# Kernel tuning notes

Measured on AMD Instinct MI355X. Metric: run time of the kernel, lower is better.

The kernel has to match this reference:

```python
import jax, jax.numpy as jnp
import numpy as np

EPS = 1e-3  # keras LayerNormalization default epsilon


def _ln(x, g, b):
    m = jnp.mean(x, axis=-1, keepdims=True)
    v = jnp.mean(jnp.square(x - m), axis=-1, keepdims=True)
    return (x - m) * jax.lax.rsqrt(v + EPS) * g + b


def setup_inputs() -> dict:
    key = jax.random.key(0)
    B, T, C, H = 64, 256, 1024, 16
    D = C // H
    ks = jax.random.split(key, 16)
    s = 0.02
    return {
        "x": jax.random.normal(ks[0], (B, T, C), jnp.float32),
        # per-head q/k/v projections (no bias), stacked over heads [H, C, D]
        "wq": jax.random.normal(ks[1], (H, C, D), jnp.float32) * s,
        "wk": jax.random.normal(ks[2], (H, C, D), jnp.float32) * s,
        "wv": jax.random.normal(ks[3], (H, C, D), jnp.float32) * s,
        "w_proj": jax.random.normal(ks[4], (C, C), jnp.float32) * s,
        "b_proj": jnp.zeros((C,), jnp.float32),
        # FFN: C -> 4C (relu) -> C
        "w1": jax.random.normal(ks[5], (C, 4 * C), jnp.float32) * s,
        "b1": jnp.zeros((4 * C,), jnp.float32),
        "w2": jax.random.normal(ks[6], (4 * C, C), jnp.float32) * s,
        "b2": jnp.zeros((C,), jnp.float32),
        # LayerNorm params: ln1 (pre-attn), ln2 (pre-ffn), ln3 (inside FeedForward)
        "g1": jnp.ones((C,), jnp.float32), "be1": jnp.zeros((C,), jnp.float32),
        "g2": jnp.ones((C,), jnp.float32), "be2": jnp.zeros((C,), jnp.float32),
        "g3": jnp.ones((C,), jnp.float32), "be3": jnp.zeros((C,), jnp.float32),
    }


def reference(x, wq, wk, wv, w_proj, b_proj, w1, b1, w2, b2,
              g1, be1, g2, be2, g3, be3):
    B, T, C = x.shape
    # --- multi-head causal self-attention on LN1(x) ---
    h = _ln(x, g1, be1)
    q = jnp.einsum('btc,hcd->bhtd', h, wq)
    k = jnp.einsum('btc,hcd->bhtd', h, wk)
    v = jnp.einsum('btc,hcd->bhtd', h, wv)
    # NOTE: original scales by C**-0.5 with C = n_embd (full dim), not head_size
    scores = jnp.einsum('bhtd,bhsd->bhts', q, k) * (C ** -0.5)
    causal = jnp.tril(jnp.ones((T, T), dtype=bool))
    scores = jnp.where(causal, scores, -jnp.inf)
    attn = jax.nn.softmax(scores, axis=-1)  # dropout is identity at inference
    out = jnp.einsum('bhts,bhsd->bhtd', attn, v)
    out = out.transpose(0, 2, 1, 3).reshape(B, T, C)  # concat heads
    out = out @ w_proj + b_proj
    x = x + out
    # --- FeedForward block (contains its own residual + LayerNorm) ---
    y = _ln(x, g2, be2)
    z = jax.nn.relu(y @ w1 + b1) @ w2 + b2
    return x + _ln(y + z, g3, be3)
```

## Files before the change

kernel.cpp:

```cpp
#include <hip/hip_runtime.h>

typedef __bf16 bf16_t;
typedef __bf16 bf16x8 __attribute__((ext_vector_type(8)));
typedef float f32x4 __attribute__((ext_vector_type(4)));

#define LN_EPS 1e-3f

__device__ __forceinline__ void gload_lds16(const void* g, void* l) {
    __builtin_amdgcn_global_load_lds(
        (__attribute__((address_space(1))) void*)(g),
        (__attribute__((address_space(3))) void*)(l), 16, 0, 0);
}

__global__ __launch_bounds__(256)
void transpose_f32_bf16(const float* __restrict__ in, bf16_t* __restrict__ outp,
                        int ldi, int ldo)
{
    __shared__ float tile[64][65];
    const int k0 = blockIdx.x * 64, n0 = blockIdx.y * 64;
    const int tid = threadIdx.x;
    const int r = tid >> 2;
    const int q = tid & 3;
    const float* src = in + (long)(k0 + r) * ldi + n0 + q * 16;
#pragma unroll
    for (int j = 0; j < 4; ++j) {
        float4 v = *(const float4*)(src + j * 4);
        tile[r][q * 16 + j * 4 + 0] = v.x;
        tile[r][q * 16 + j * 4 + 1] = v.y;
        tile[r][q * 16 + j * 4 + 2] = v.z;
        tile[r][q * 16 + j * 4 + 3] = v.w;
    }
    __syncthreads();
    union { bf16_t e[16]; uint4 u[2]; } pk;
#pragma unroll
    for (int j = 0; j < 16; ++j) pk.e[j] = (bf16_t)tile[q * 16 + j][r];
    bf16_t* dst = outp + (long)(n0 + r) * ldo + k0 + q * 16;
    *(uint4*)(dst)     = pk.u[0];
    *(uint4*)(dst + 8) = pk.u[1];
}

__global__ __launch_bounds__(256)
void pack_qkv_t(const float* __restrict__ wq, const float* __restrict__ wk,
                const float* __restrict__ wv, bf16_t* __restrict__ outp)
{
    __shared__ float tile[64][65];
    const int m   = blockIdx.y;
    const int sel = m >> 4, h = m & 15;
    const float* in = ((sel == 0) ? wq : (sel == 1) ? wk : wv) + (long)h * 65536;
    bf16_t* out = outp + ((long)sel * 1024 + h * 64) * 1024;
    const int k0 = blockIdx.x * 64;
    const int tid = threadIdx.x;
    const int r = tid >> 2;
    const int q = tid & 3;
    const float* src = in + (long)(k0 + r) * 64 + q * 16;
#pragma unroll
    for (int j = 0; j < 4; ++j) {
        float4 v = *(const float4*)(src + j * 4);
        tile[r][q * 16 + j * 4 + 0] = v.x;
        tile[r][q * 16 + j * 4 + 1] = v.y;
        tile[r][q * 16 + j * 4 + 2] = v.z;
        tile[r][q * 16 + j * 4 + 3] = v.w;
    }
    __syncthreads();
    union { bf16_t e[16]; uint4 u[2]; } pk;
#pragma unroll
    for (int j = 0; j < 16; ++j) pk.e[j] = (bf16_t)tile[q * 16 + j][r];
    bf16_t* dst = out + (long)r * 1024 + k0 + q * 16;
    *(uint4*)(dst)     = pk.u[0];
    *(uint4*)(dst + 8) = pk.u[1];
}

__global__ __launch_bounds__(256)
void ln_fwd(const float* __restrict__ in, const float* __restrict__ g,
            const float* __restrict__ be, bf16_t* __restrict__ outp)
{
    const long row = blockIdx.x;
    const int t = threadIdx.x;
    float4 v = ((const float4*)(in + row * 1024))[t];
    float s  = v.x + v.y + v.z + v.w;
    float sq = v.x * v.x + v.y * v.y + v.z * v.z + v.w * v.w;
#pragma unroll
    for (int off = 1; off < 64; off <<= 1) {
        s  += __shfl_xor(s, off);
        sq += __shfl_xor(sq, off);
    }
    __shared__ float red[8];
    if ((t & 63) == 0) { red[(t >> 6) * 2] = s; red[(t >> 6) * 2 + 1] = sq; }
    __syncthreads();
    s  = red[0] + red[2] + red[4] + red[6];
    sq = red[1] + red[3] + red[5] + red[7];
    float mean = s * 0.0009765625f;
    float var  = sq * 0.0009765625f - mean * mean;
    float rstd = rsqrtf(var + LN_EPS);
    float4 gv = ((const float4*)g)[t];
    float4 bv = ((const float4*)be)[t];
    union { bf16_t h[4]; uint2 u; } pk;
    pk.h[0] = (bf16_t)((v.x - mean) * rstd * gv.x + bv.x);
    pk.h[1] = (bf16_t)((v.y - mean) * rstd * gv.y + bv.y);
    pk.h[2] = (bf16_t)((v.z - mean) * rstd * gv.z + bv.z);
    pk.h[3] = (bf16_t)((v.w - mean) * rstd * gv.w + bv.w);
    *(uint2*)(outp + row * 1024 + t * 4) = pk.u;
}

__global__ __launch_bounds__(256)
void ln3_kernel(const bf16_t* __restrict__ in, const float* __restrict__ g,
                const float* __restrict__ be, float* outp, const float* res)
{
    const long row = blockIdx.x;
    const int t = threadIdx.x;
    union { uint2 u; bf16_t h[4]; } pk;
    pk.u = *(const uint2*)(in + row * 1024 + t * 4);
    float v0 = (float)pk.h[0], v1 = (float)pk.h[1], v2 = (float)pk.h[2], v3 = (float)pk.h[3];
    float s  = v0 + v1 + v2 + v3;
    float sq = v0 * v0 + v1 * v1 + v2 * v2 + v3 * v3;
#pragma unroll
    for (int off = 1; off < 64; off <<= 1) {
        s  += __shfl_xor(s, off);
        sq += __shfl_xor(sq, off);
    }
    __shared__ float red[8];
    if ((t & 63) == 0) { red[(t >> 6) * 2] = s; red[(t >> 6) * 2 + 1] = sq; }
    __syncthreads();
    s  = red[0] + red[2] + red[4] + red[6];
    sq = red[1] + red[3] + red[5] + red[7];
    float mean = s * 0.0009765625f;
    float var  = sq * 0.0009765625f - mean * mean;
    float rstd = rsqrtf(var + LN_EPS);
    float4 gv = ((const float4*)g)[t];
    float4 bv = ((const float4*)be)[t];
    float4 rv = ((const float4*)(res + row * 1024))[t];
    float4 ov;
    ov.x = rv.x + (v0 - mean) * rstd * gv.x + bv.x;
    ov.y = rv.y + (v1 - mean) * rstd * gv.y + bv.y;
    ov.z = rv.z + (v2 - mean) * rstd * gv.z + bv.z;
    ov.w = rv.w + (v3 - mean) * rstd * gv.w + bv.w;
    ((float4*)outp)[row * 256 + t] = ov;
}

template<int MODE>
__global__ __launch_bounds__(512, 2)
void gemm_bt(const bf16_t* __restrict__ Ap, const bf16_t* __restrict__ Bp,
             void* outp, const float* __restrict__ bias,
             const void* addp, int M, int N, int K)
{
    __shared__ __attribute__((aligned(16))) bf16_t As0[256 * 64];
    __shared__ __attribute__((aligned(16))) bf16_t As1[256 * 64];
    __shared__ __attribute__((aligned(16))) bf16_t As2[256 * 64];
    __shared__ __attribute__((aligned(16))) bf16_t Bs0[256 * 64];
    __shared__ __attribute__((aligned(16))) bf16_t Bs1[256 * 64];

    const int tid  = threadIdx.x;
    const int w    = tid >> 6, lane = tid & 63;
    const int l16  = lane & 15, lg = lane >> 4;
    const int wm   = w >> 2, wn = w & 3;
    const int srow = lane >> 3;
    const int sslot = lane & 7;

    const int gx  = gridDim.x;
    const int gy  = gridDim.y;
    const int nwg = gx * gy;
    const int bid = blockIdx.y * gx + blockIdx.x;
    const int cpx = nwg >> 3;
    const int sid = (bid & 7) * cpx + (bid >> 3);
    const long m0 = (long)(sid / gy) * 256;
    const long n0 = (long)(sid % gy) * 256;
    const int nkt = K >> 6;

    f32x4 acc[8][4] = {};
    bf16x8 a[4][2], b0[2][2], b1[2][2];

    auto STAGEH = [&](const bf16_t* src, long row0, int kt, bf16_t* dst, int h) {
#pragma unroll
        for (int i = 0; i < 2; ++i) {
            int r  = h * 128 + w * 16 + i * 8 + srow;
            int ss = sslot ^ (r & 7);
            gload_lds16(src + (row0 + r) * (long)K + (long)kt * 64 + ss * 8,
                        dst + (h * 128 + w * 16 + i * 8) * 64);
        }
    };

#define LDA_M(buf, mh) do {                                               \
    _Pragma("unroll") for (int j = 0; j < 4; ++j)                         \
    _Pragma("unroll") for (int kk = 0; kk < 2; ++kk) {                    \
        int r  = wm * 128 + (mh) * 64 + j * 16 + l16;                     \
        int ss = (kk * 4 + lg) ^ (r & 7);                                 \
        a[j][kk] = *(const bf16x8*)&buf[r * 64 + ss * 8];                 \
    } } while (0)

#define LDB_M(dst, buf, nh) do {                                          \
    _Pragma("unroll") for (int n = 0; n < 2; ++n)                         \
    _Pragma("unroll") for (int kk = 0; kk < 2; ++kk) {                    \
        int r  = wn * 64 + ((nh) * 2 + n) * 16 + l16;                     \
        int ss = (kk * 4 + lg) ^ (r & 7);                                 \
        dst[n][kk] = *(const bf16x8*)&buf[r * 64 + ss * 8];               \
    } } while (0)

#define MMA_M(bv, mh, nh) do {                                            \
    __builtin_amdgcn_s_setprio(1);                                        \
    _Pragma("unroll") for (int j = 0; j < 4; ++j)                         \
    _Pragma("unroll") for (int n = 0; n < 2; ++n)                         \
    _Pragma("unroll") for (int kk = 0; kk < 2; ++kk)                      \
        acc[(mh) * 4 + j][(nh) * 2 + n] =                                 \
            __builtin_amdgcn_mfma_f32_16x16x32_bf16(                      \
                a[j][kk], bv[n][kk], acc[(mh) * 4 + j][(nh) * 2 + n],     \
                0, 0, 0);                                                 \
    __builtin_amdgcn_s_setprio(0);                                        \
} while (0)

#define PRE_MFMA() do { __builtin_amdgcn_s_barrier();                     \
    asm volatile("s_waitcnt lgkmcnt(0)" ::: "memory");                    \
    __builtin_amdgcn_sched_barrier(0); } while (0)

    STAGEH(Ap, m0, 0, As0, 0); STAGEH(Ap, m0, 0, As0, 1);
    STAGEH(Bp, n0, 0, Bs0, 0); STAGEH(Bp, n0, 0, Bs0, 1);
    if (nkt > 1) { STAGEH(Ap, m0, 1, As1, 0); STAGEH(Ap, m0, 1, As1, 1); }
    asm volatile("s_waitcnt vmcnt(0)" ::: "memory");
    __builtin_amdgcn_s_barrier();
    __builtin_amdgcn_sched_barrier(0);

    bf16_t *Ar = As0, *An1 = As1, *An2 = As2;
    bf16_t *Br = Bs0, *Bw = Bs1;

    for (int c = 0; c < nkt; ++c) {
        const bool pfa = (c + 2 < nkt);
        const bool pfb = (c + 1 < nkt);

        LDA_M(Ar, 0); LDB_M(b0, Br, 0);
        if (pfb) { STAGEH(Bp, n0, c + 1, Bw, 0); STAGEH(Bp, n0, c + 1, Bw, 1); }
        if (pfa) STAGEH(Ap, m0, c + 2, An2, 0);
        PRE_MFMA(); MMA_M(b0, 0, 0); __builtin_amdgcn_s_barrier();
        LDB_M(b1, Br, 1);
        PRE_MFMA(); MMA_M(b1, 0, 1); __builtin_amdgcn_s_barrier();
        LDA_M(Ar, 1);
        if (pfa) STAGEH(Ap, m0, c + 2, An2, 1);
        PRE_MFMA(); MMA_M(b1, 1, 1); __builtin_amdgcn_s_barrier();
        if (pfa) { asm volatile("s_waitcnt vmcnt(4)" ::: "memory"); }
        else     { asm volatile("s_waitcnt vmcnt(0)" ::: "memory"); }
        __builtin_amdgcn_s_barrier();
        __builtin_amdgcn_sched_barrier(0);
        MMA_M(b0, 1, 0); __builtin_amdgcn_s_barrier();

        bf16_t* t = Ar; Ar = An1; An1 = An2; An2 = t;
        t = Br; Br = Bw; Bw = t;
    }

#pragma unroll
    for (int fm = 0; fm < 8; ++fm) {
#pragma unroll
        for (int fn = 0; fn < 4; ++fn) {
            const long gcol = n0 + wn * 64 + fn * 16 + l16;
            float bv = 0.f;
            if (MODE != 0 && MODE != 4) bv = bias[gcol];
            const long grow0 = m0 + wm * 128 + fm * 16 + lg * 4;
            if (MODE == 4 && gcol >= 2048) {
                union { bf16_t h[4]; uint2 u; } pk;
#pragma unroll
                for (int e = 0; e < 4; ++e) pk.h[e] = (bf16_t)acc[fm][fn][e];
                const int hh = (int)(gcol >> 6) - 32;
                const int d  = (int)gcol & 63;
                const long bb = grow0 >> 8;
                const int s0  = (int)grow0 & 255;
                *(uint2*)((bf16_t*)addp + ((bb * 16 + hh) * 64 + d) * 256 + s0) = pk.u;
                continue;
            }
#pragma unroll
            for (int e = 0; e < 4; ++e) {
                const long grow = grow0 + e;
                float v = acc[fm][fn][e];
                if (MODE == 0 || MODE == 4) {
                    ((bf16_t*)outp)[grow * N + gcol] = (bf16_t)v;
                } else if (MODE == 1) {
                    v += bv + ((const float*)addp)[grow * N + gcol];
                    ((float*)outp)[grow * N + gcol] = v;
                } else if (MODE == 2) {
                    v += bv; v = v > 0.f ? v : 0.f;
                    ((bf16_t*)outp)[grow * N + gcol] = (bf16_t)v;
                } else {
                    v += bv + (float)((const bf16_t*)addp)[grow * N + gcol];
                    ((bf16_t*)outp)[grow * N + gcol] = (bf16_t)v;
                }
            }
        }
    }
#undef LDA_M
#undef LDB_M
#undef MMA_M
#undef PRE_MFMA
}

__global__ __launch_bounds__(256)
void attn_kernel(const bf16_t* __restrict__ qkv, const bf16_t* __restrict__ vt,
                 bf16_t* __restrict__ outp)
{
    __shared__ __attribute__((aligned(16))) bf16_t Kt[4][64 * 64];
    __shared__ __attribute__((aligned(16))) bf16_t Vt[4][64 * 64];
    __shared__ __attribute__((aligned(16))) bf16_t Ps[4][16 * 72];

    const int tid = threadIdx.x, w = tid >> 6, lane = tid & 63;
    const int l16 = lane & 15, lg = lane >> 4;
    const int b = blockIdx.x >> 4, hh = blockIdx.x & 15;
    const bf16_t* pq = qkv + (long)(b * 256) * 3072 + hh * 64;
    const bf16_t* pv = vt + (long)blockIdx.x * 64 * 256;
    const int sr8 = lane >> 3;
    const int sl  = lane & 7;

    bf16x8 qf[4][2];
#pragma unroll
    for (int fm = 0; fm < 4; ++fm)
#pragma unroll
        for (int kk = 0; kk < 2; ++kk)
            qf[fm][kk] = *(const bf16x8*)(pq + (long)(fm * 64 + w * 16 + l16) * 3072
                                          + kk * 32 + lg * 8);

#pragma unroll
    for (int st = 0; st < 4; ++st)
#pragma unroll
        for (int i = 0; i < 2; ++i) {
            int r  = w * 16 + i * 8 + sr8;
            int ss = sl ^ (r & 7);
            gload_lds16(pq + (long)(st * 64 + r) * 3072 + 1024 + ss * 8,
                        &Kt[st][(w * 16 + i * 8) * 64]);
            gload_lds16(pv + (long)r * 256 + st * 64 + ss * 8,
                        &Vt[st][(w * 16 + i * 8) * 64]);
        }
    asm volatile("s_waitcnt vmcnt(0)" ::: "memory");
    __syncthreads();

    f32x4 o[4][4] = {};
    float mrun[4][4], lrun[4][4];
#pragma unroll
    for (int i = 0; i < 4; ++i)
#pragma unroll
        for (int j = 0; j < 4; ++j) { mrun[i][j] = -__builtin_inff(); lrun[i][j] = 0.f; }

#pragma unroll
    for (int st = 0; st < 4; ++st) {
        f32x4 s[4][4] = {};
#pragma unroll
        for (int ks = 0; ks < 2; ++ks) {
            bf16x8 kb[4];
#pragma unroll
            for (int fs = 0; fs < 4; ++fs)
                kb[fs] = *(const bf16x8*)&Kt[st][(fs * 16 + l16) * 64
                                                + ((ks * 4 + lg) ^ (l16 & 7)) * 8];
#pragma unroll
            for (int fm = 0; fm < 4; ++fm) {
                if (fm < st) continue;
#pragma unroll
                for (int fs = 0; fs < 4; ++fs)
                    s[fm][fs] = __builtin_amdgcn_mfma_f32_16x16x32_bf16(
                        qf[fm][ks], kb[fs], s[fm][fs], 0, 0, 0);
            }
        }

#pragma unroll
        for (int fm = 0; fm < 4; ++fm) {
            if (fm < st) continue;
#pragma unroll
            for (int fs = 0; fs < 4; ++fs)
#pragma unroll
                for (int e = 0; e < 4; ++e) {
                    float v = s[fm][fs][e] * 0.03125f;
                    if (st == fm && (fs * 16 + l16) > (w * 16 + lg * 4 + e))
                        v = -__builtin_inff();
                    s[fm][fs][e] = v;
                }
#pragma unroll
            for (int e = 0; e < 4; ++e) {
                float pm = fmaxf(fmaxf(s[fm][0][e], s[fm][1][e]),
                                 fmaxf(s[fm][2][e], s[fm][3][e]));
#pragma unroll
                for (int off = 1; off < 16; off <<= 1) pm = fmaxf(pm, __shfl_xor(pm, off));
                float mnew  = fmaxf(mrun[fm][e], pm);
                float alpha = __expf(mrun[fm][e] - mnew);
                float rs = 0.f;
#pragma unroll
                for (int fs = 0; fs < 4; ++fs) {
                    float p = __expf(s[fm][fs][e] - mnew);
                    s[fm][fs][e] = p;
                    rs += p;
                }
#pragma unroll
                for (int off = 1; off < 16; off <<= 1) rs += __shfl_xor(rs, off);
                lrun[fm][e] = lrun[fm][e] * alpha + rs;
                mrun[fm][e] = mnew;
#pragma unroll
                for (int fd = 0; fd < 4; ++fd) o[fm][fd][e] *= alpha;
            }
#pragma unroll
            for (int fs = 0; fs < 4; ++fs)
#pragma unroll
                for (int e = 0; e < 4; ++e)
                    Ps[w][(lg * 4 + e) * 72 + fs * 16 + l16] = (bf16_t)s[fm][fs][e];
            bf16x8 ap0 = *(const bf16x8*)&Ps[w][l16 * 72 + lg * 8];
            bf16x8 ap1 = *(const bf16x8*)&Ps[w][l16 * 72 + 32 + lg * 8];
#pragma unroll
            for (int fd = 0; fd < 4; ++fd) {
                bf16x8 vb0 = *(const bf16x8*)&Vt[st][(fd * 16 + l16) * 64
                                                    + ((lg) ^ (l16 & 7)) * 8];
                bf16x8 vb1 = *(const bf16x8*)&Vt[st][(fd * 16 + l16) * 64
                                                    + ((4 + lg) ^ (l16 & 7)) * 8];
                o[fm][fd] = __builtin_amdgcn_mfma_f32_16x16x32_bf16(ap0, vb0, o[fm][fd], 0, 0, 0);
                o[fm][fd] = __builtin_amdgcn_mfma_f32_16x16x32_bf16(ap1, vb1, o[fm][fd], 0, 0, 0);
            }
        }
    }

#pragma unroll
    for (int fm = 0; fm < 4; ++fm)
#pragma unroll
        for (int e = 0; e < 4; ++e) {
            float inv = 1.f / lrun[fm][e];
            long row = (long)b * 256 + fm * 64 + w * 16 + lg * 4 + e;
#pragma unroll
            for (int fd = 0; fd < 4; ++fd)
                outp[row * 1024 + hh * 64 + fd * 16 + l16] =
                    (bf16_t)(o[fm][fd][e] * inv);
        }
}

extern "C" void kernel_launch(void* const* d_in, const int* in_sizes, int n_in,
                              void* d_out, int out_size, void* d_ws, size_t ws_size,
                              hipStream_t stream)
{
    (void)in_sizes; (void)n_in; (void)out_size; (void)ws_size;
    const float* x      = (const float*)d_in[0];
    const float* wq     = (const float*)d_in[1];
    const float* wk     = (const float*)d_in[2];
    const float* wv     = (const float*)d_in[3];
    const float* w_proj = (const float*)d_in[4];
    const float* b_proj = (const float*)d_in[5];
    const float* w1     = (const float*)d_in[6];
    const float* b1     = (const float*)d_in[7];
    const float* w2     = (const float*)d_in[8];
    const float* b2     = (const float*)d_in[9];
    const float* g1  = (const float*)d_in[10]; const float* be1 = (const float*)d_in[11];
    const float* g2  = (const float*)d_in[12]; const float* be2 = (const float*)d_in[13];
    const float* g3  = (const float*)d_in[14]; const float* be3 = (const float*)d_in[15];

    char* ws = (char*)d_ws;
    bf16_t* wqkv  = (bf16_t*)(ws + 0);
    bf16_t* wproj = (bf16_t*)(ws + 6291456);
    bf16_t* w1t   = (bf16_t*)(ws + 8388608);
    bf16_t* w2t   = (bf16_t*)(ws + 16777216);
    bf16_t* h     = (bf16_t*)(ws + 25165824);
    bf16_t* qkv   = (bf16_t*)(ws + 58720256);
    bf16_t* attn  = h;
    bf16_t* u     = h;
    bf16_t* y     = (bf16_t*)(ws + 159383552);
    bf16_t* vt    = y;
    float*  x2    = (float*)d_out;
    bf16_t* tbuf  = y;

    const int M = 16384;

    transpose_f32_bf16<<<dim3(16, 16), 256, 0, stream>>>(w_proj, wproj, 1024, 1024);
    transpose_f32_bf16<<<dim3(16, 64), 256, 0, stream>>>(w1, w1t, 4096, 1024);
    transpose_f32_bf16<<<dim3(64, 16), 256, 0, stream>>>(w2, w2t, 1024, 4096);
    pack_qkv_t<<<dim3(16, 48), 256, 0, stream>>>(wq, wk, wv, wqkv);

    ln_fwd<<<M, 256, 0, stream>>>(x, g1, be1, h);
    gemm_bt<4><<<dim3(64, 12), 512, 0, stream>>>(h, wqkv, qkv, nullptr, vt, M, 3072, 1024);
    attn_kernel<<<1024, 256, 0, stream>>>(qkv, vt, attn);
    gemm_bt<1><<<dim3(64, 4), 512, 0, stream>>>(attn, wproj, x2, b_proj, x, M, 1024, 1024);
    ln_fwd<<<M, 256, 0, stream>>>(x2, g2, be2, y);
    gemm_bt<2><<<dim3(64, 16), 512, 0, stream>>>(y, w1t, u, b1, nullptr, M, 4096, 1024);
    gemm_bt<3><<<dim3(64, 4), 512, 0, stream>>>(u, w2t, tbuf, b2, y, M, 1024, 4096);
    ln3_kernel<<<M, 256, 0, stream>>>(tbuf, g3, be3, (float*)d_out, x2);
}
```

Before: 623.4 us.

## Merge weight-prep kernels, store residual x2 in bf16, and reorder A prefetch

The four weight transpose/pack launches become one prep_w kernel that picks its tile from the block index. When the workspace is big enough, the attention-projection GEMM writes the residual sum x2 as bf16 into workspace rather than fp32 into the output. New bf16-input LN and LN3 variants then read it, cutting memory traffic for the mid-block residual. Separately, the second-half A prefetch in the GEMM main loop is issued one MFMA phase earlier to overlap it better. Keeping the residual in bf16 lowers the precision of the skip connection added to the final output.

```diff
diff --git a/kernel.cpp b/kernel.cpp
--- a/kernel.cpp
+++ b/kernel.cpp
@@ -12,62 +12,55 @@
         (__attribute__((address_space(3))) void*)(l), 16, 0, 0);
 }
 
-__global__ __launch_bounds__(256)
-void transpose_f32_bf16(const float* __restrict__ in, bf16_t* __restrict__ outp,
-                        int ldi, int ldo)
-{
-    __shared__ float tile[64][65];
-    const int k0 = blockIdx.x * 64, n0 = blockIdx.y * 64;
+__device__ __forceinline__ void tile_tr(const float* in, long ldi,
+                                        bf16_t* out, long ldo,
+                                        int k0, int n0, float* tile)
+{
     const int tid = threadIdx.x;
-    const int r = tid >> 2;
-    const int q = tid & 3;
+    const int r = tid >> 2, q = tid & 3;
     const float* src = in + (long)(k0 + r) * ldi + n0 + q * 16;
 #pragma unroll
     for (int j = 0; j < 4; ++j) {
         float4 v = *(const float4*)(src + j * 4);
-        tile[r][q * 16 + j * 4 + 0] = v.x;
-        tile[r][q * 16 + j * 4 + 1] = v.y;
-        tile[r][q * 16 + j * 4 + 2] = v.z;
-        tile[r][q * 16 + j * 4 + 3] = v.w;
+        tile[r * 65 + q * 16 + j * 4 + 0] = v.x;
+        tile[r * 65 + q * 16 + j * 4 + 1] = v.y;
+        tile[r * 65 + q * 16 + j * 4 + 2] = v.z;
+        tile[r * 65 + q * 16 + j * 4 + 3] = v.w;
     }
     __syncthreads();
     union { bf16_t e[16]; uint4 u[2]; } pk;
 #pragma unroll
-    for (int j = 0; j < 16; ++j) pk.e[j] = (bf16_t)tile[q * 16 + j][r];
-    bf16_t* dst = outp + (long)(n0 + r) * ldo + k0 + q * 16;
+    for (int j = 0; j < 16; ++j) pk.e[j] = (bf16_t)tile[(q * 16 + j) * 65 + r];
+    bf16_t* dst = out + (long)(n0 + r) * ldo + k0 + q * 16;
     *(uint4*)(dst)     = pk.u[0];
     *(uint4*)(dst + 8) = pk.u[1];
 }
 
 __global__ __launch_bounds__(256)
-void pack_qkv_t(const float* __restrict__ wq, const float* __restrict__ wk,
-                const float* __restrict__ wv, bf16_t* __restrict__ outp)
-{
-    __shared__ float tile[64][65];
-    const int m   = blockIdx.y;
-    const int sel = m >> 4, h = m & 15;
-    const float* in = ((sel == 0) ? wq : (sel == 1) ? wk : wv) + (long)h * 65536;
-    bf16_t* out = outp + ((long)sel * 1024 + h * 64) * 1024;
-    const int k0 = blockIdx.x * 64;
-    const int tid = threadIdx.x;
-    const int r = tid >> 2;
-    const int q = tid & 3;
-    const float* src = in + (long)(k0 + r) * 64 + q * 16;
-#pragma unroll
-    for (int j = 0; j < 4; ++j) {
-        float4 v = *(const float4*)(src + j * 4);
-        tile[r][q * 16 + j * 4 + 0] = v.x;
-        tile[r][q * 16 + j * 4 + 1] = v.y;
-        tile[r][q * 16 + j * 4 + 2] = v.z;
-        tile[r][q * 16 + j * 4 + 3] = v.w;
-    }
-    __syncthreads();
-    union { bf16_t e[16]; uint4 u[2]; } pk;
-#pragma unroll
-    for (int j = 0; j < 16; ++j) pk.e[j] = (bf16_t)tile[q * 16 + j][r];
-    bf16_t* dst = out + (long)r * 1024 + k0 + q * 16;
-    *(uint4*)(dst)     = pk.u[0];
-    *(uint4*)(dst + 8) = pk.u[1];
+void prep_w(const float* __restrict__ wq, const float* __restrict__ wk,
+            const float* __restrict__ wv, const float* __restrict__ w_proj,
+            const float* __restrict__ w1, const float* __restrict__ w2,
+            bf16_t* __restrict__ wqkv, bf16_t* __restrict__ wproj,
+            bf16_t* __restrict__ w1t, bf16_t* __restrict__ w2t)
+{
+    __shared__ float tile[64 * 65];
+    int id = blockIdx.x;
+    if (id < 256) {
+        tile_tr(w_proj, 1024, wproj, 1024, (id & 15) * 64, (id >> 4) * 64, tile);
+    } else if (id < 1280) {
+        int t = id - 256;
+        tile_tr(w1, 4096, w1t, 1024, (t & 15) * 64, (t >> 4) * 64, tile);
+    } else if (id < 2304) {
+        int t = id - 1280;
+        tile_tr(w2, 1024, w2t, 4096, (t & 63) * 64, (t >> 6) * 64, tile);
+    } else {
+        int t = id - 2304;
+        int m = t >> 4, kx = t & 15;
+        int sel = m >> 4, h = m & 15;
+        const float* in = ((sel == 0) ? wq : (sel == 1) ? wk : wv) + (long)h * 65536;
+        bf16_t* out = wqkv + ((long)sel * 1024 + h * 64) * 1024;
+        tile_tr(in, 64, out, 1024, kx * 64, 0, tile);
+    }
 }
 
 __global__ __launch_bounds__(256)
@@ -103,14 +96,15 @@
 }
 
 __global__ __launch_bounds__(256)
-void ln3_kernel(const bf16_t* __restrict__ in, const float* __restrict__ g,
-                const float* __restrict__ be, float* outp, const float* res)
+void ln_fwd_b(const bf16_t* __restrict__ in, const float* __restrict__ g,
+              const float* __restrict__ be, bf16_t* __restrict__ outp)
 {
     const long row = blockIdx.x;
     const int t = threadIdx.x;
-    union { uint2 u; bf16_t h[4]; } pk;
-    pk.u = *(const uint2*)(in + row * 1024 + t * 4);
-    float v0 = (float)pk.h[0], v1 = (float)pk.h[1], v2 = (float)pk.h[2], v3 = (float)pk.h[3];
+    union { uint2 u; bf16_t h[4]; } pin;
+    pin.u = *(const uint2*)(in + row * 1024 + t * 4);
+    float v0 = (float)pin.h[0], v1 = (float)pin.h[1],
+          v2 = (float)pin.h[2], v3 = (float)pin.h[3];
     float s  = v0 + v1 + v2 + v3;
     float sq = v0 * v0 + v1 * v1 + v2 * v2 + v3 * v3;
 #pragma unroll
@@ -128,12 +122,56 @@
     float rstd = rsqrtf(var + LN_EPS);
     float4 gv = ((const float4*)g)[t];
     float4 bv = ((const float4*)be)[t];
-    float4 rv = ((const float4*)(res + row * 1024))[t];
+    union { bf16_t h[4]; uint2 u; } pk;
+    pk.h[0] = (bf16_t)((v0 - mean) * rstd * gv.x + bv.x);
+    pk.h[1] = (bf16_t)((v1 - mean) * rstd * gv.y + bv.y);
+    pk.h[2] = (bf16_t)((v2 - mean) * rstd * gv.z + bv.z);
+    pk.h[3] = (bf16_t)((v3 - mean) * rstd * gv.w + bv.w);
+    *(uint2*)(outp + row * 1024 + t * 4) = pk.u;
+}
+
+template<int RESB>
+__global__ __launch_bounds__(256)
+void ln3_kernel(const bf16_t* __restrict__ in, const float* __restrict__ g,
+                const float* __restrict__ be, float* outp, const void* res)
+{
+    const long row = blockIdx.x;
+    const int t = threadIdx.x;
+    union { uint2 u; bf16_t h[4]; } pk;
+    pk.u = *(const uint2*)(in + row * 1024 + t * 4);
+    float v0 = (float)pk.h[0], v1 = (float)pk.h[1], v2 = (float)pk.h[2], v3 = (float)pk.h[3];
+    float s  = v0 + v1 + v2 + v3;
+    float sq = v0 * v0 + v1 * v1 + v2 * v2 + v3 * v3;
+#pragma unroll
+    for (int off = 1; off < 64; off <<= 1) {
+        s  += __shfl_xor(s, off);
+        sq += __shfl_xor(sq, off);
+    }
+    __shared__ float red[8];
+    if ((t & 63) == 0) { red[(t >> 6) * 2] = s; red[(t >> 6) * 2 + 1] = sq; }
+    __syncthreads();
+    s  = red[0] + red[2] + red[4] + red[6];
+    sq = red[1] + red[3] + red[5] + red[7];
+    float mean = s * 0.0009765625f;
+    float var  = sq * 0.0009765625f - mean * mean;
+    float rstd = rsqrtf(var + LN_EPS);
+    float4 gv = ((const float4*)g)[t];
+    float4 bv = ((const float4*)be)[t];
+    float r0, r1, r2, r3;
+    if (RESB == 0) {
+        float4 rv = ((const float4*)((const float*)res + row * 1024))[t];
+        r0 = rv.x; r1 = rv.y; r2 = rv.z; r3 = rv.w;
+    } else {
+        union { uint2 u; bf16_t h[4]; } pr;
+        pr.u = *(const uint2*)((const bf16_t*)res + row * 1024 + t * 4);
+        r0 = (float)pr.h[0]; r1 = (float)pr.h[1];
+        r2 = (float)pr.h[2]; r3 = (float)pr.h[3];
+    }
     float4 ov;
-    ov.x = rv.x + (v0 - mean) * rstd * gv.x + bv.x;
-    ov.y = rv.y + (v1 - mean) * rstd * gv.y + bv.y;
-    ov.z = rv.z + (v2 - mean) * rstd * gv.z + bv.z;
-    ov.w = rv.w + (v3 - mean) * rstd * gv.w + bv.w;
+    ov.x = r0 + (v0 - mean) * rstd * gv.x + bv.x;
+    ov.y = r1 + (v1 - mean) * rstd * gv.y + bv.y;
+    ov.z = r2 + (v2 - mean) * rstd * gv.z + bv.z;
+    ov.w = r3 + (v3 - mean) * rstd * gv.w + bv.w;
     ((float4*)outp)[row * 256 + t] = ov;
 }
 
@@ -230,9 +268,9 @@
         if (pfa) STAGEH(Ap, m0, c + 2, An2, 0);
         PRE_MFMA(); MMA_M(b0, 0, 0); __builtin_amdgcn_s_barrier();
         LDB_M(b1, Br, 1);
+        if (pfa) STAGEH(Ap, m0, c + 2, An2, 1);
         PRE_MFMA(); MMA_M(b1, 0, 1); __builtin_amdgcn_s_barrier();
         LDA_M(Ar, 1);
-        if (pfa) STAGEH(Ap, m0, c + 2, An2, 1);
         PRE_MFMA(); MMA_M(b1, 1, 1); __builtin_amdgcn_s_barrier();
         if (pfa) { asm volatile("s_waitcnt vmcnt(4)" ::: "memory"); }
         else     { asm volatile("s_waitcnt vmcnt(0)" ::: "memory"); }
@@ -275,8 +313,11 @@
                 } else if (MODE == 2) {
                     v += bv; v = v > 0.f ? v : 0.f;
                     ((bf16_t*)outp)[grow * N + gcol] = (bf16_t)v;
+                } else if (MODE == 3) {
+                    v += bv + (float)((const bf16_t*)addp)[grow * N + gcol];
+                    ((bf16_t*)outp)[grow * N + gcol] = (bf16_t)v;
                 } else {
-                    v += bv + (float)((const bf16_t*)addp)[grow * N + gcol];
+                    v += bv + ((const float*)addp)[grow * N + gcol];
                     ((bf16_t*)outp)[grow * N + gcol] = (bf16_t)v;
                 }
             }
@@ -423,7 +464,7 @@
                               void* d_out, int out_size, void* d_ws, size_t ws_size,
                               hipStream_t stream)
 {
-    (void)in_sizes; (void)n_in; (void)out_size; (void)ws_size;
+    (void)in_sizes; (void)n_in; (void)out_size;
     const float* x      = (const float*)d_in[0];
     const float* wq     = (const float*)d_in[1];
     const float* wk     = (const float*)d_in[2];
@@ -449,22 +490,31 @@
     bf16_t* u     = h;
     bf16_t* y     = (bf16_t*)(ws + 159383552);
     bf16_t* vt    = y;
-    float*  x2    = (float*)d_out;
     bf16_t* tbuf  = y;
+    bf16_t* x2b   = (bf16_t*)(ws + 192937984);
+    const bool big = ws_size >= (size_t)226492416;
 
     const int M = 16384;
 
-    transpose_f32_bf16<<<dim3(16, 16), 256, 0, stream>>>(w_proj, wproj, 1024, 1024);
-    transpose_f32_bf16<<<dim3(16, 64), 256, 0, stream>>>(w1, w1t, 4096, 1024);
-    transpose_f32_bf16<<<dim3(64, 16), 256, 0, stream>>>(w2, w2t, 1024, 4096);
-    pack_qkv_t<<<dim3(16, 48), 256, 0, stream>>>(wq, wk, wv, wqkv);
+    prep_w<<<3072, 256, 0, stream>>>(wq, wk, wv, w_proj, w1, w2,
+                                     wqkv, wproj, w1t, w2t);
 
     ln_fwd<<<M, 256, 0, stream>>>(x, g1, be1, h);
     gemm_bt<4><<<dim3(64, 12), 512, 0, stream>>>(h, wqkv, qkv, nullptr, vt, M, 3072, 1024);
     attn_kernel<<<1024, 256, 0, stream>>>(qkv, vt, attn);
-    gemm_bt<1><<<dim3(64, 4), 512, 0, stream>>>(attn, wproj, x2, b_proj, x, M, 1024, 1024);
-    ln_fwd<<<M, 256, 0, stream>>>(x2, g2, be2, y);
-    gemm_bt<2><<<dim3(64, 16), 512, 0, stream>>>(y, w1t, u, b1, nullptr, M, 4096, 1024);
-    gemm_bt<3><<<dim3(64, 4), 512, 0, stream>>>(u, w2t, tbuf, b2, y, M, 1024, 4096);
-    ln3_kernel<<<M, 256, 0, stream>>>(tbuf, g3, be3, (float*)d_out, x2);
-}
+
+    if (big) {
+        gemm_bt<5><<<dim3(64, 4), 512, 0, stream>>>(attn, wproj, x2b, b_proj, x, M, 1024, 1024);
+        ln_fwd_b<<<M, 256, 0, stream>>>(x2b, g2, be2, y);
+        gemm_bt<2><<<dim3(64, 16), 512, 0, stream>>>(y, w1t, u, b1, nullptr, M, 4096, 1024);
+        gemm_bt<3><<<dim3(64, 4), 512, 0, stream>>>(u, w2t, tbuf, b2, y, M, 1024, 4096);
+        ln3_kernel<1><<<M, 256, 0, stream>>>(tbuf, g3, be3, (float*)d_out, x2b);
+    } else {
+        float* x2 = (float*)d_out;
+        gemm_bt<1><<<dim3(64, 4), 512, 0, stream>>>(attn, wproj, x2, b_proj, x, M, 1024, 1024);
+        ln_fwd<<<M, 256, 0, stream>>>(x2, g2, be2, y);
+        gemm_bt<2><<<dim3(64, 16), 512, 0, stream>>>(y, w1t, u, b1, nullptr, M, 4096, 1024);
+        gemm_bt<3><<<dim3(64, 4), 512, 0, stream>>>(u, w2t, tbuf, b2, y, M, 1024, 4096);
+        ln3_kernel<0><<<M, 256, 0, stream>>>(tbuf, g3, be3, (float*)d_out, x2);
+    }
+}
```

Result: faster. 601.7 us (-3.5%).
